# Performance work log

Measured on AMD Instinct MI355X. Metric: run time of the kernel, lower is better.

The kernel has to match this reference:

```python
import jax, jax.numpy as jnp
import numpy as np

B, N, M = 2048, 4096, 4096


def setup_inputs() -> dict:
    key = jax.random.key(0)
    kt, kv, kr = jax.random.split(key, 3)
    # sorted abscissae per sample (interp1d assumes monotone t)
    t = jnp.sort(jax.random.uniform(kt, (B, N), dtype=jnp.float32), axis=-1)
    v = jax.random.normal(kv, (B, N), dtype=jnp.float32)
    # queries slightly outside [0,1] to exercise the extrapolation clamp
    r = jax.random.uniform(kr, (B, M), minval=-0.05, maxval=1.05, dtype=jnp.float32)
    return {"t": t, "v": v, "r": r}


def _interp1(t, v, r):
    # t: [N] sorted, v: [N], r: [M]
    idx = jnp.clip(jnp.searchsorted(t, r, side='right'), 1, t.shape[0] - 1)
    t0 = t[idx - 1]
    t1 = t[idx]
    v0 = v[idx - 1]
    v1 = v[idx]
    denom = jnp.where(t1 == t0, jnp.float32(1.0), t1 - t0)
    out = v0 + (r - t0) / denom * (v1 - v0)
    # scipy fill_value=(v[0], v[-1]) with bounds_error=False: clamp extrapolation
    out = jnp.where(r < t[0], v[0], out)
    out = jnp.where(r > t[-1], v[-1], out)
    return out


def reference(t, v, r):
    # batched 1D linear interpolation with clamped extrapolation -> [B, M]
    return jax.vmap(_interp1)(t, v, r)
```

## Files before the change

kernel.cpp:

```cpp
#include <hip/hip_runtime.h>

constexpr int B = 2048;
constexpr int N = 4096;
constexpr int M = 4096;
constexpr int K = 2048;

__global__ __launch_bounds__(256) void interp_kernel(
    const float* __restrict__ t,
    const float* __restrict__ v,
    const float* __restrict__ r,
    float* __restrict__ out) {
    __shared__ float2 stv[N];
    __shared__ int lut[K];

    const int b = blockIdx.x;
    const float* tb = t + (size_t)b * N;
    const float* vb = v + (size_t)b * N;
    const float* rb = r + (size_t)b * M;
    float* ob = out + (size_t)b * M;

    for (int i = threadIdx.x; i < N / 4; i += blockDim.x) {
        const float4 t4 = ((const float4*)tb)[i];
        const float4 v4 = ((const float4*)vb)[i];
        stv[4 * i + 0] = make_float2(t4.x, v4.x);
        stv[4 * i + 1] = make_float2(t4.y, v4.y);
        stv[4 * i + 2] = make_float2(t4.z, v4.z);
        stv[4 * i + 3] = make_float2(t4.w, v4.w);
    }
    for (int k = threadIdx.x; k < K; k += blockDim.x) lut[k] = N;
    __syncthreads();

    for (int j = threadIdx.x; j < N; j += blockDim.x) {
        const float tj = stv[j].x;
        int khi = (int)(tj * K);
        if (khi > K - 1) khi = K - 1;
        int klo = 0;
        if (j > 0) klo = (int)(stv[j - 1].x * K) + 1;
        for (int k = klo; k <= khi; ++k) lut[k] = j;
    }
    __syncthreads();

    const float tfirst = stv[0].x;
    const float vfirst = stv[0].y;
    const float tlast = stv[N - 1].x;
    const float vlast = stv[N - 1].y;

    const float4* r4 = (const float4*)rb;
    float4* o4 = (float4*)ob;
    for (int base = 0; base < M / 4; base += 2 * 256) {
        const int ia = base + threadIdx.x;
        const int ib = ia + 256;
        const float4 qa = r4[ia];
        const float4 qb = r4[ib];
        float q[8] = {qa.x, qa.y, qa.z, qa.w, qb.x, qb.y, qb.z, qb.w};
        int lo[8], hi[8];

        #pragma unroll
        for (int j = 0; j < 8; ++j) {
            int k = (int)(q[j] * K);
            k = k < 0 ? 0 : (k > K - 1 ? K - 1 : k);
            lo[j] = lut[k];
            hi[j] = (k == K - 1) ? N : lut[k + 1];
        }
        #pragma unroll
        for (int j = 0; j < 8; ++j) {
            #pragma unroll
            for (int s = 0; s < 3; ++s) {
                const int safe = lo[j] < N - 1 ? lo[j] : N - 1;
                const bool adv = (lo[j] < hi[j]) && (stv[safe].x <= q[j]);
                lo[j] += adv ? 1 : 0;
            }
            while (lo[j] < hi[j] && stv[lo[j]].x <= q[j]) ++lo[j];
        }
        float o[8];
        #pragma unroll
        for (int j = 0; j < 8; ++j) {
            const int idx = lo[j] < 1 ? 1 : (lo[j] > N - 1 ? N - 1 : lo[j]);
            const float2 p0 = stv[idx - 1];
            const float2 p1 = stv[idx];
            const float denom = (p1.x == p0.x) ? 1.0f : (p1.x - p0.x);
            float oo = p0.y + (q[j] - p0.x) / denom * (p1.y - p0.y);
            oo = (q[j] < tfirst) ? vfirst : oo;
            oo = (q[j] > tlast) ? vlast : oo;
            o[j] = oo;
        }
        o4[ia] = make_float4(o[0], o[1], o[2], o[3]);
        o4[ib] = make_float4(o[4], o[5], o[6], o[7]);
    }
}

extern "C" void kernel_launch(void* const* d_in, const int* in_sizes, int n_in,
                              void* d_out, int out_size, void* d_ws, size_t ws_size,
                              hipStream_t stream) {
    const float* t = (const float*)d_in[0];
    const float* v = (const float*)d_in[1];
    const float* r = (const float*)d_in[2];
    float* out = (float*)d_out;
    interp_kernel<<<B, 256, 0, stream>>>(t, v, r, out);
}
```

Before: 151.5 us.

## Shrink LDS footprint: keep only t in shared, read v from global

```diff
diff --git a/kernel.cpp b/kernel.cpp
--- a/kernel.cpp
+++ b/kernel.cpp
@@ -5,13 +5,13 @@
 constexpr int M = 4096;
 constexpr int K = 2048;
 
-__global__ __launch_bounds__(256) void interp_kernel(
+__global__ __launch_bounds__(256, 8) void interp_kernel(
     const float* __restrict__ t,
     const float* __restrict__ v,
     const float* __restrict__ r,
     float* __restrict__ out) {
-    __shared__ float2 stv[N];
-    __shared__ int lut[K];
+    __shared__ float st[N];
+    __shared__ unsigned short lut[K];
 
     const int b = blockIdx.x;
     const float* tb = t + (size_t)b * N;
@@ -20,30 +20,24 @@
     float* ob = out + (size_t)b * M;
 
     for (int i = threadIdx.x; i < N / 4; i += blockDim.x) {
-        const float4 t4 = ((const float4*)tb)[i];
-        const float4 v4 = ((const float4*)vb)[i];
-        stv[4 * i + 0] = make_float2(t4.x, v4.x);
-        stv[4 * i + 1] = make_float2(t4.y, v4.y);
-        stv[4 * i + 2] = make_float2(t4.z, v4.z);
-        stv[4 * i + 3] = make_float2(t4.w, v4.w);
+        ((float4*)st)[i] = ((const float4*)tb)[i];
     }
-    for (int k = threadIdx.x; k < K; k += blockDim.x) lut[k] = N;
+    for (int k = threadIdx.x; k < K; k += blockDim.x) lut[k] = (unsigned short)N;
     __syncthreads();
 
     for (int j = threadIdx.x; j < N; j += blockDim.x) {
-        const float tj = stv[j].x;
-        int khi = (int)(tj * K);
+        int khi = (int)(st[j] * K);
         if (khi > K - 1) khi = K - 1;
         int klo = 0;
-        if (j > 0) klo = (int)(stv[j - 1].x * K) + 1;
-        for (int k = klo; k <= khi; ++k) lut[k] = j;
+        if (j > 0) klo = (int)(st[j - 1] * K) + 1;
+        for (int k = klo; k <= khi; ++k) lut[k] = (unsigned short)j;
     }
     __syncthreads();
 
-    const float tfirst = stv[0].x;
-    const float vfirst = stv[0].y;
-    const float tlast = stv[N - 1].x;
-    const float vlast = stv[N - 1].y;
+    const float tfirst = st[0];
+    const float tlast = st[N - 1];
+    const float vfirst = vb[0];
+    const float vlast = vb[N - 1];
 
     const float4* r4 = (const float4*)rb;
     float4* o4 = (float4*)ob;
@@ -60,26 +54,28 @@
             int k = (int)(q[j] * K);
             k = k < 0 ? 0 : (k > K - 1 ? K - 1 : k);
             lo[j] = lut[k];
-            hi[j] = (k == K - 1) ? N : lut[k + 1];
+            hi[j] = (k == K - 1) ? N : (int)lut[k + 1];
         }
         #pragma unroll
         for (int j = 0; j < 8; ++j) {
             #pragma unroll
-            for (int s = 0; s < 3; ++s) {
+            for (int s = 0; s < 2; ++s) {
                 const int safe = lo[j] < N - 1 ? lo[j] : N - 1;
-                const bool adv = (lo[j] < hi[j]) && (stv[safe].x <= q[j]);
+                const bool adv = (lo[j] < hi[j]) && (st[safe] <= q[j]);
                 lo[j] += adv ? 1 : 0;
             }
-            while (lo[j] < hi[j] && stv[lo[j]].x <= q[j]) ++lo[j];
+            while (lo[j] < hi[j] && st[lo[j]] <= q[j]) ++lo[j];
         }
         float o[8];
         #pragma unroll
         for (int j = 0; j < 8; ++j) {
             const int idx = lo[j] < 1 ? 1 : (lo[j] > N - 1 ? N - 1 : lo[j]);
-            const float2 p0 = stv[idx - 1];
-            const float2 p1 = stv[idx];
-            const float denom = (p1.x == p0.x) ? 1.0f : (p1.x - p0.x);
-            float oo = p0.y + (q[j] - p0.x) / denom * (p1.y - p0.y);
+            const float t0 = st[idx - 1];
+            const float t1 = st[idx];
+            const float v0 = vb[idx - 1];
+            const float v1 = vb[idx];
+            const float denom = (t1 == t0) ? 1.0f : (t1 - t0);
+            float oo = v0 + (q[j] - t0) / denom * (v1 - v0);
             oo = (q[j] < tfirst) ? vfirst : oo;
             oo = (q[j] > tlast) ? vlast : oo;
             o[j] = oo;
```

Result: slower. 163.7 us (+8.0%).

## Prefetch queries before table build, shrink LUT to ushort, process 16 queries per thread

Applied to the files above, without the earlier changes.

```diff
diff --git a/kernel.cpp b/kernel.cpp
--- a/kernel.cpp
+++ b/kernel.cpp
@@ -4,14 +4,15 @@
 constexpr int N = 4096;
 constexpr int M = 4096;
 constexpr int K = 2048;
+constexpr int QPT = 16;
 
-__global__ __launch_bounds__(256) void interp_kernel(
+__global__ __launch_bounds__(256, 4) void interp_kernel(
     const float* __restrict__ t,
     const float* __restrict__ v,
     const float* __restrict__ r,
     float* __restrict__ out) {
     __shared__ float2 stv[N];
-    __shared__ int lut[K];
+    __shared__ unsigned short lut[K + 2];
 
     const int b = blockIdx.x;
     const float* tb = t + (size_t)b * N;
@@ -19,7 +20,12 @@
     const float* rb = r + (size_t)b * M;
     float* ob = out + (size_t)b * M;
 
-    for (int i = threadIdx.x; i < N / 4; i += blockDim.x) {
+    const float4* r4 = (const float4*)rb;
+    float4 qv[QPT / 4];
+    #pragma unroll
+    for (int p = 0; p < QPT / 4; ++p) qv[p] = r4[threadIdx.x + 256 * p];
+
+    for (int i = threadIdx.x; i < N / 4; i += 256) {
         const float4 t4 = ((const float4*)tb)[i];
         const float4 v4 = ((const float4*)vb)[i];
         stv[4 * i + 0] = make_float2(t4.x, v4.x);
@@ -27,16 +33,15 @@
         stv[4 * i + 2] = make_float2(t4.z, v4.z);
         stv[4 * i + 3] = make_float2(t4.w, v4.w);
     }
-    for (int k = threadIdx.x; k < K; k += blockDim.x) lut[k] = N;
+    for (int k = threadIdx.x; k <= K; k += 256) lut[k] = (unsigned short)N;
     __syncthreads();
 
-    for (int j = threadIdx.x; j < N; j += blockDim.x) {
-        const float tj = stv[j].x;
-        int khi = (int)(tj * K);
+    for (int j = threadIdx.x; j < N; j += 256) {
+        int khi = (int)(stv[j].x * K);
         if (khi > K - 1) khi = K - 1;
         int klo = 0;
         if (j > 0) klo = (int)(stv[j - 1].x * K) + 1;
-        for (int k = klo; k <= khi; ++k) lut[k] = j;
+        for (int k = klo; k <= khi; ++k) lut[k] = (unsigned short)j;
     }
     __syncthreads();
 
@@ -45,47 +50,50 @@
     const float tlast = stv[N - 1].x;
     const float vlast = stv[N - 1].y;
 
-    const float4* r4 = (const float4*)rb;
+    float q[QPT];
+    #pragma unroll
+    for (int p = 0; p < QPT / 4; ++p) {
+        q[4 * p + 0] = qv[p].x;
+        q[4 * p + 1] = qv[p].y;
+        q[4 * p + 2] = qv[p].z;
+        q[4 * p + 3] = qv[p].w;
+    }
+
+    int lo[QPT], hi[QPT];
+    #pragma unroll
+    for (int j = 0; j < QPT; ++j) {
+        int k = (int)(q[j] * K);
+        k = k < 0 ? 0 : (k > K - 1 ? K - 1 : k);
+        lo[j] = (int)lut[k];
+        hi[j] = (int)lut[k + 1];
+    }
+    #pragma unroll
+    for (int j = 0; j < QPT; ++j) {
+        #pragma unroll
+        for (int s = 0; s < 2; ++s) {
+            const int safe = lo[j] < N - 1 ? lo[j] : N - 1;
+            const bool adv = (lo[j] < hi[j]) && (stv[safe].x <= q[j]);
+            lo[j] += adv ? 1 : 0;
+        }
+        while (lo[j] < hi[j] && stv[lo[j]].x <= q[j]) ++lo[j];
+    }
+    float o[QPT];
+    #pragma unroll
+    for (int j = 0; j < QPT; ++j) {
+        const int idx = lo[j] < 1 ? 1 : (lo[j] > N - 1 ? N - 1 : lo[j]);
+        const float2 p0 = stv[idx - 1];
+        const float2 p1 = stv[idx];
+        const float denom = (p1.x == p0.x) ? 1.0f : (p1.x - p0.x);
+        float oo = p0.y + (q[j] - p0.x) / denom * (p1.y - p0.y);
+        oo = (q[j] < tfirst) ? vfirst : oo;
+        oo = (q[j] > tlast) ? vlast : oo;
+        o[j] = oo;
+    }
     float4* o4 = (float4*)ob;
-    for (int base = 0; base < M / 4; base += 2 * 256) {
-        const int ia = base + threadIdx.x;
-        const int ib = ia + 256;
-        const float4 qa = r4[ia];
-        const float4 qb = r4[ib];
-        float q[8] = {qa.x, qa.y, qa.z, qa.w, qb.x, qb.y, qb.z, qb.w};
-        int lo[8], hi[8];
-
-        #pragma unroll
-        for (int j = 0; j < 8; ++j) {
-            int k = (int)(q[j] * K);
-            k = k < 0 ? 0 : (k > K - 1 ? K - 1 : k);
-            lo[j] = lut[k];
-            hi[j] = (k == K - 1) ? N : lut[k + 1];
-        }
-        #pragma unroll
-        for (int j = 0; j < 8; ++j) {
-            #pragma unroll
-            for (int s = 0; s < 3; ++s) {
-                const int safe = lo[j] < N - 1 ? lo[j] : N - 1;
-                const bool adv = (lo[j] < hi[j]) && (stv[safe].x <= q[j]);
-                lo[j] += adv ? 1 : 0;
-            }
-            while (lo[j] < hi[j] && stv[lo[j]].x <= q[j]) ++lo[j];
-        }
-        float o[8];
-        #pragma unroll
-        for (int j = 0; j < 8; ++j) {
-            const int idx = lo[j] < 1 ? 1 : (lo[j] > N - 1 ? N - 1 : lo[j]);
-            const float2 p0 = stv[idx - 1];
-            const float2 p1 = stv[idx];
-            const float denom = (p1.x == p0.x) ? 1.0f : (p1.x - p0.x);
-            float oo = p0.y + (q[j] - p0.x) / denom * (p1.y - p0.y);
-            oo = (q[j] < tfirst) ? vfirst : oo;
-            oo = (q[j] > tlast) ? vlast : oo;
-            o[j] = oo;
-        }
-        o4[ia] = make_float4(o[0], o[1], o[2], o[3]);
-        o4[ib] = make_float4(o[4], o[5], o[6], o[7]);
+    #pragma unroll
+    for (int p = 0; p < QPT / 4; ++p) {
+        o4[threadIdx.x + 256 * p] =
+            make_float4(o[4 * p + 0], o[4 * p + 1], o[4 * p + 2], o[4 * p + 3]);
     }
 }
 
```

After: 156.8 us. +3.5%, slower.
